# Performance work log

Measured on AMD Instinct MI355X. Metric: run time of the kernel, lower is better.

## Reference

```python
import jax, jax.numpy as jnp
import numpy as np
import math

EPS = 1e-6
N_HEADS = 16
THETA = 10000.0


def rms(x):
    # parameter-free RMSNorm: x * rsqrt(mean(x^2) + eps)
    return x * jax.lax.rsqrt(jnp.mean(x * x, axis=-1, keepdims=True) + EPS)


def silu(x):
    return x * jax.nn.sigmoid(x)


def rope_cos_sin(T, head_dim, theta):
    inv = 1.0 / (theta ** (jnp.arange(0, head_dim, 2, dtype=jnp.float32) / head_dim))
    freqs = jnp.arange(T, dtype=jnp.float32)[:, None] * inv[None, :]  # (T, head_dim/2)
    return jnp.cos(freqs), jnp.sin(freqs)


def apply_rope(x, cos, sin):
    # x: (B, H, T, dh); even/odd interleaved pairs as in torch reshape(...,-1,2).unbind(-1)
    x1 = x[..., 0::2]
    x2 = x[..., 1::2]
    o1 = x1 * cos - x2 * sin
    o2 = x1 * sin + x2 * cos
    return jnp.stack([o1, o2], axis=-1).reshape(x.shape)


def cache_linear(x, down, up):
    # x: (B,T,in), down: (h,in,c), up: (h,out,c) -> (B,T,out)
    a = jnp.einsum('bti,hic->bthc', x, down)
    a = jnp.einsum('bthc,hoc->btho', a, up)
    return rms(jnp.prod(a, axis=2))


def setup_inputs() -> dict:
    key = jax.random.key(0)
    ks = jax.random.split(key, 10)
    B, T, D = 1, 2048, 1024
    d_ff, ncb, cdim = 4096, 4, 64
    lin_std = math.sqrt(2.0 / (D + D))
    return {
        'x': jax.random.normal(ks[0], (B, T, D), jnp.float32),
        'ln1_w': jnp.ones((D,), jnp.float32),
        'ln2_w': jnp.ones((D,), jnp.float32),
        'wq': jax.random.normal(ks[1], (D, D), jnp.float32) * lin_std,
        'wk': jax.random.normal(ks[2], (D, D), jnp.float32) * lin_std,
        'wv': jax.random.normal(ks[3], (D, D), jnp.float32) * lin_std,
        'wo': jax.random.normal(ks[4], (D, D), jnp.float32) * lin_std,
        'w1_down': jax.random.normal(ks[5], (ncb, D, cdim), jnp.float32) * math.sqrt(2.0 / (D + cdim)),
        'w1_up': jax.random.normal(ks[6], (ncb, d_ff, cdim), jnp.float32) * math.sqrt(2.0 / (d_ff + cdim)),
        'w2_down': jax.random.normal(ks[7], (ncb, d_ff, cdim), jnp.float32) * math.sqrt(2.0 / (d_ff + cdim)),
        'w2_up': jax.random.normal(ks[8], (ncb, D, cdim), jnp.float32) * math.sqrt(2.0 / (D + cdim)),
    }


def reference(x, ln1_w, ln2_w, wq, wk, wv, wo, w1_down, w1_up, w2_down, w2_up):
    B, T, D = x.shape
    H = N_HEADS
    dh = D // H

    # --- attention sublayer (pre-RMSNorm) ---
    h = rms(x) * ln1_w
    def proj(w):
        return (h @ w.T).reshape(B, T, H, dh).transpose(0, 2, 1, 3)  # (B,H,T,dh)
    q, k, v = proj(wq), proj(wk), proj(wv)

    cos, sin = rope_cos_sin(T, dh, THETA)  # (T, dh/2)
    q = apply_rope(q, cos, sin)
    k = apply_rope(k, cos, sin)

    scores = jnp.einsum('bhid,bhjd->bhij', q, k) / math.sqrt(dh)
    causal = jnp.tril(jnp.ones((T, T), dtype=bool))
    scores = jnp.where(causal, scores, -jnp.inf)
    attn = jax.nn.softmax(scores, axis=-1)
    o = jnp.einsum('bhij,bhjd->bhid', attn, v)
    o = o.transpose(0, 2, 1, 3).reshape(B, T, D) @ wo.T
    x = x + o

    # --- CacheSiLU FFN sublayer (pre-RMSNorm) ---
    h2 = rms(x) * ln2_w
    a = cache_linear(h2, w1_down, w1_up)   # (B,T,d_ff)
    f = cache_linear(silu(a), w2_down, w2_up)  # (B,T,D)
    return x + f
```

## Files before the change

### kernel.cpp

```cpp
#include <hip/hip_runtime.h>
#include <math.h>
#include <stdint.h>

#define T_LEN   2048
#define D_MODEL 1024
#define NH      16
#define DFF     4096

typedef __attribute__((ext_vector_type(8))) short bf16x8;
typedef __attribute__((ext_vector_type(4))) float f32x4;
typedef __attribute__((ext_vector_type(4))) unsigned short u16x4;
typedef __attribute__((ext_vector_type(8))) unsigned short u16x8;
typedef unsigned short u16;

__device__ inline u16 f2b(float x) {
  unsigned int u = __float_as_uint(x);
  unsigned int r = (u + 0x7fffu + ((u >> 16) & 1u)) >> 16;
  return (u16)r;
}
__device__ inline float b2f(u16 h) { return __uint_as_float(((unsigned int)h) << 16); }

typedef const __attribute__((address_space(1))) unsigned int* gas_t;
typedef __attribute__((address_space(3))) unsigned int* las_t;
__device__ inline void gl_lds16(const void* g, void* l) {
  __builtin_amdgcn_global_load_lds((gas_t)g, (las_t)l, 16, 0, 0);
}

#define MFMA16(a, b, c) __builtin_amdgcn_mfma_f32_16x16x32_bf16((a), (b), (c), 0, 0, 0)

__global__ __launch_bounds__(256) void conv_bf16_kernel(
    const float* __restrict__ src, u16* __restrict__ dst, int n4) {
  int i = blockIdx.x * 256 + threadIdx.x;
  if (i < n4) {
    float4 v = reinterpret_cast<const float4*>(src)[i];
    u16x4 o = {f2b(v.x), f2b(v.y), f2b(v.z), f2b(v.w)};
    reinterpret_cast<u16x4*>(dst)[i] = o;
  }
}

__global__ __launch_bounds__(256) void conv4_kernel(
    const float* s0, const float* s1, const float* s2, const float* s3,
    u16* d0, u16* d1, u16* d2, u16* d3, int n4) {
  int z = blockIdx.z;
  const float* s = z == 0 ? s0 : (z == 1 ? s1 : (z == 2 ? s2 : s3));
  u16* d = z == 0 ? d0 : (z == 1 ? d1 : (z == 2 ? d2 : d3));
  int i = blockIdx.x * 256 + threadIdx.x;
  if (i < n4) {
    float4 v = reinterpret_cast<const float4*>(s)[i];
    u16x4 o = {f2b(v.x), f2b(v.y), f2b(v.z), f2b(v.w)};
    reinterpret_cast<u16x4*>(d)[i] = o;
  }
}

__global__ __launch_bounds__(256) void tr_kernel(
    const float* __restrict__ w, u16* __restrict__ wt, int K) {
  int k0 = blockIdx.x * 64, h = blockIdx.y;
  __shared__ float Ts[64][65];
  int tid = threadIdx.x;
#pragma unroll
  for (int i = 0; i < 4; ++i) {
    int idx = tid + i * 256;
    int r = idx >> 4, c4 = (idx & 15) * 4;
    float4 v = *reinterpret_cast<const float4*>(w + ((size_t)h * K + k0 + r) * 64 + c4);
    Ts[r][c4 + 0] = v.x; Ts[r][c4 + 1] = v.y; Ts[r][c4 + 2] = v.z; Ts[r][c4 + 3] = v.w;
  }
  __syncthreads();
#pragma unroll
  for (int i = 0; i < 4; ++i) {
    int idx = tid + i * 256;
    int c = idx >> 4, k4 = (idx & 15) * 4;
    u16x4 o = {f2b(Ts[k4 + 0][c]), f2b(Ts[k4 + 1][c]), f2b(Ts[k4 + 2][c]), f2b(Ts[k4 + 3][c])};
    *reinterpret_cast<u16x4*>(wt + (size_t)(h * 64 + c) * K + k0 + k4) = o;
  }
}

__global__ __launch_bounds__(256) void vtrans_kernel(
    const u16* __restrict__ V, u16* __restrict__ VT) {
  __shared__ u16 Ts[64][72];
  int t0 = blockIdx.x * 64, h = blockIdx.y;
  int tid = threadIdx.x;
#pragma unroll
  for (int it = 0; it < 2; ++it) {
    int c = tid + it * 256;
    int t = c >> 3, d8 = (c & 7) * 8;
    *reinterpret_cast<u16x8*>(&Ts[t][d8]) =
        *reinterpret_cast<const u16x8*>(V + (size_t)(t0 + t) * D_MODEL + h * 64 + d8);
  }
  __syncthreads();
#pragma unroll
  for (int it = 0; it < 2; ++it) {
    int c = tid + it * 256;
    int d = c >> 3, t8 = (c & 7) * 8;
    u16x8 o;
#pragma unroll
    for (int j = 0; j < 8; ++j) o[j] = Ts[t8 + j][d];
    *reinterpret_cast<u16x8*>(VT + ((size_t)h * 64 + d) * T_LEN + t0 + t8) = o;
  }
}

template <int NV, bool WEIGHT>
__global__ __launch_bounds__(256) void rms_bf16_kernel(
    const float* __restrict__ in, const float* __restrict__ w,
    u16* __restrict__ out, int width) {
  int row = blockIdx.x, tid = threadIdx.x;
  const float* rp = in + (size_t)row * width;
  float4 vals[NV];
  float ss = 0.f;
#pragma unroll
  for (int v = 0; v < NV; ++v) {
    vals[v] = reinterpret_cast<const float4*>(rp)[v * 256 + tid];
    ss += vals[v].x * vals[v].x + vals[v].y * vals[v].y +
          vals[v].z * vals[v].z + vals[v].w * vals[v].w;
  }
  for (int off = 32; off; off >>= 1) ss += __shfl_down(ss, off, 64);
  __shared__ float wsum[4];
  if ((tid & 63) == 0) wsum[tid >> 6] = ss;
  __syncthreads();
  float tot = wsum[0] + wsum[1] + wsum[2] + wsum[3];
  float scale = rsqrtf(tot / (float)width + 1e-6f);
#pragma unroll
  for (int v = 0; v < NV; ++v) {
    int c4 = v * 256 + tid;
    float o0 = vals[v].x * scale, o1 = vals[v].y * scale,
          o2 = vals[v].z * scale, o3 = vals[v].w * scale;
    if constexpr (WEIGHT) {
      float4 wv = reinterpret_cast<const float4*>(w)[c4];
      o0 *= wv.x; o1 *= wv.y; o2 *= wv.z; o3 *= wv.w;
    }
    u16x4 ov = {f2b(o0), f2b(o1), f2b(o2), f2b(o3)};
    reinterpret_cast<u16x4*>(out + (size_t)row * width)[c4] = ov;
  }
}

__global__ __launch_bounds__(256) void rms_silu_bf16_kernel(
    const u16* __restrict__ in, u16* __restrict__ out) {
  int row = blockIdx.x, tid = threadIdx.x;
  const u16* rp = in + (size_t)row * DFF;
  float f[16];
  float ss = 0.f;
#pragma unroll
  for (int v = 0; v < 2; ++v) {
    u16x8 c = reinterpret_cast<const u16x8*>(rp)[v * 256 + tid];
#pragma unroll
    for (int j = 0; j < 8; ++j) {
      float x = b2f((u16)c[j]);
      f[v * 8 + j] = x;
      ss += x * x;
    }
  }
  for (int off = 32; off; off >>= 1) ss += __shfl_down(ss, off, 64);
  __shared__ float wsum[4];
  if ((tid & 63) == 0) wsum[tid >> 6] = ss;
  __syncthreads();
  float tot = wsum[0] + wsum[1] + wsum[2] + wsum[3];
  float scale = rsqrtf(tot / (float)DFF + 1e-6f);
#pragma unroll
  for (int v = 0; v < 2; ++v) {
    u16x8 o;
#pragma unroll
    for (int j = 0; j < 8; ++j) {
      float x = f[v * 8 + j] * scale;
      x = x / (1.f + __expf(-x));
      o[j] = f2b(x);
    }
    reinterpret_cast<u16x8*>(out + (size_t)row * DFF)[v * 256 + tid] = o;
  }
}

__global__ __launch_bounds__(256) void rms_add_kernel(
    const float* __restrict__ in, const float* __restrict__ res,
    float* __restrict__ out) {
  int row = blockIdx.x, tid = threadIdx.x;
  float4 v = reinterpret_cast<const float4*>(in + (size_t)row * D_MODEL)[tid];
  float ss = v.x * v.x + v.y * v.y + v.z * v.z + v.w * v.w;
  for (int off = 32; off; off >>= 1) ss += __shfl_down(ss, off, 64);
  __shared__ float wsum[4];
  if ((tid & 63) == 0) wsum[tid >> 6] = ss;
  __syncthreads();
  float tot = wsum[0] + wsum[1] + wsum[2] + wsum[3];
  float scale = rsqrtf(tot / (float)D_MODEL + 1e-6f);
  float4 rv = reinterpret_cast<const float4*>(res + (size_t)row * D_MODEL)[tid];
  float4 o = make_float4(v.x * scale + rv.x, v.y * scale + rv.y,
                         v.z * scale + rv.z, v.w * scale + rv.w);
  reinterpret_cast<float4*>(out + (size_t)row * D_MODEL)[tid] = o;
}

template <int OUT>
__device__ inline void gemm_nt_body(const u16* A, const u16* B, void* Cv,
                                    const float* RES, int N, int lda, int Kloop,
                                    int row0, int col0) {
  __shared__ __align__(16) u16 As[128 * 32];
  __shared__ __align__(16) u16 Bs[128 * 32];
  int tid = threadIdx.x, lane = tid & 63, wid = tid >> 6;
  int wr = wid >> 1, wc = wid & 1;
  const f32x4 fz = {0.f, 0.f, 0.f, 0.f};
  f32x4 acc[4][4];
#pragma unroll
  for (int m = 0; m < 4; ++m)
#pragma unroll
    for (int n = 0; n < 4; ++n) acc[m][n] = fz;

  for (int k0 = 0; k0 < Kloop; k0 += 32) {
    __syncthreads();
#pragma unroll
    for (int i = 0; i < 2; ++i) {
      int wl = wid * 2 + i;
      int row = wl * 16 + (lane >> 2);
      int col8 = ((lane & 3) ^ (row & 3)) * 8;
      gl_lds16(A + (size_t)(row0 + row) * lda + k0 + col8, &As[wl * 512]);
      gl_lds16(B + (size_t)(col0 + row) * lda + k0 + col8, &Bs[wl * 512]);
    }
    __syncthreads();
    bf16x8 af[4], bfr[4];
#pragma unroll
    for (int m = 0; m < 4; ++m) {
      int r = wr * 64 + m * 16 + (lane & 15);
      af[m] = *reinterpret_cast<const bf16x8*>(&As[r * 32 + (((lane >> 4) ^ (r & 3)) << 3)]);
    }
#pragma unroll
    for (int n = 0; n < 4; ++n) {
      int r = wc * 64 + n * 16 + (lane & 15);
      bfr[n] = *reinterpret_cast<const bf16x8*>(&Bs[r * 32 + (((lane >> 4) ^ (r & 3)) << 3)]);
    }
#pragma unroll
    for (int m = 0; m < 4; ++m)
#pragma unroll
      for (int n = 0; n < 4; ++n) acc[m][n] = MFMA16(af[m], bfr[n], acc[m][n]);
  }
#pragma unroll
  for (int m = 0; m < 4; ++m)
#pragma unroll
    for (int n = 0; n < 4; ++n)
#pragma unroll
      for (int r = 0; r < 4; ++r) {
        int grow = row0 + wr * 64 + m * 16 + (lane >> 4) * 4 + r;
        int gcol = col0 + wc * 64 + n * 16 + (lane & 15);
        float v = acc[m][n][r];
        if constexpr (OUT == 0) {
          ((u16*)Cv)[(size_t)grow * N + gcol] = f2b(v);
        } else if constexpr (OUT == 1) {
          ((float*)Cv)[(size_t)grow * N + gcol] = v + RES[(size_t)grow * N + gcol];
        } else {
          ((float*)Cv)[(size_t)grow * N + gcol] = v;
        }
      }
}

__global__ __launch_bounds__(256) void gemm_qkv_kernel(
    const u16* __restrict__ A, const u16* Bq, const u16* Bk, const u16* Bv,
    u16* Cq, u16* Ck, u16* Cvp) {
  const u16* B = blockIdx.z == 0 ? Bq : (blockIdx.z == 1 ? Bk : Bv);
  u16* C = blockIdx.z == 0 ? Cq : (blockIdx.z == 1 ? Ck : Cvp);
  gemm_nt_body<0>(A, B, C, nullptr, D_MODEL, D_MODEL, D_MODEL,
                  blockIdx.y * 128, blockIdx.x * 128);
}
__global__ __launch_bounds__(256) void gemm_res_kernel(
    const u16* __restrict__ A, const u16* __restrict__ B, float* __restrict__ C,
    const float* __restrict__ RES) {
  gemm_nt_body<1>(A, B, C, RES, D_MODEL, D_MODEL, D_MODEL,
                  blockIdx.y * 128, blockIdx.x * 128);
}
__global__ __launch_bounds__(256) void gemm_splitk_kernel(
    const u16* __restrict__ A, const u16* __restrict__ B, float* __restrict__ Cp,
    int lda, int Kchunk) {
  int z = blockIdx.z;
  gemm_nt_body<2>(A + (size_t)z * Kchunk, B + (size_t)z * Kchunk,
                  Cp + (size_t)z * (T_LEN * 256), nullptr, 256, lda, Kchunk,
                  blockIdx.y * 128, blockIdx.x * 128);
}
__global__ __launch_bounds__(256) void reduce_conv_kernel(
    const float* __restrict__ part, u16* __restrict__ out, int n4, int nsplit) {
  int i = blockIdx.x * 256 + threadIdx.x;
  if (i >= n4) return;
  float4 a = reinterpret_cast<const float4*>(part)[i];
  for (int s = 1; s < nsplit; ++s) {
    float4 b = reinterpret_cast<const float4*>(part)[i + (size_t)s * n4];
    a.x += b.x; a.y += b.y; a.z += b.z; a.w += b.w;
  }
  u16x4 o = {f2b(a.x), f2b(a.y), f2b(a.z), f2b(a.w)};
  reinterpret_cast<u16x4*>(out)[i] = o;
}

template <bool BF16_OUT>
__global__ __launch_bounds__(256) void cache_up_mfma(
    const u16* __restrict__ Acoef, const u16* __restrict__ UP,
    void* __restrict__ Gv, int N) {
  __shared__ __align__(16) u16 As[128 * 64];
  __shared__ __align__(16) u16 Bs[128 * 64];
  int tid = threadIdx.x, lane = tid & 63, wid = tid >> 6;
  int wr = wid >> 1, wc = wid & 1;
  int row0 = blockIdx.y * 128, col0 = blockIdx.x * 128;
  const f32x4 fz = {0.f, 0.f, 0.f, 0.f};
  f32x4 prod[4][4];
#pragma unroll
  for (int m = 0; m < 4; ++m)
#pragma unroll
    for (int n = 0; n < 4; ++n) prod[m][n] = fz + 1.f;

  for (int h = 0; h < 4; ++h) {
    __syncthreads();
#pragma unroll
    for (int i = 0; i < 4; ++i) {
      int wl = wid * 4 + i;
      int row = wl * 8 + (lane >> 3);
      int col8 = ((lane & 7) ^ (row & 7)) * 8;
      gl_lds16(Acoef + (size_t)(row0 + row) * 256 + h * 64 + col8, &As[wl * 512]);
      gl_lds16(UP + ((size_t)h * N + col0 + row) * 64 + col8, &Bs[wl * 512]);
    }
    __syncthreads();
    f32x4 d[4][4];
#pragma unroll
    for (int m = 0; m < 4; ++m)
#pragma unroll
      for (int n = 0; n < 4; ++n) d[m][n] = fz;
#pragma unroll
    for (int kh = 0; kh < 2; ++kh) {
      bf16x8 af[4], bfr[4];
#pragma unroll
      for (int m = 0; m < 4; ++m) {
        int r = wr * 64 + m * 16 + (lane & 15);
        int slot = kh * 4 + (lane >> 4);
        af[m] = *reinterpret_cast<const bf16x8*>(&As[r * 64 + ((slot ^ (r & 7)) << 3)]);
      }
#pragma unroll
      for (int n = 0; n < 4; ++n) {
        int r = wc * 64 + n * 16 + (lane & 15);
        int slot = kh * 4 + (lane >> 4);
        bfr[n] = *reinterpret_cast<const bf16x8*>(&Bs[r * 64 + ((slot ^ (r & 7)) << 3)]);
      }
#pragma unroll
      for (int m = 0; m < 4; ++m)
#pragma unroll
        for (int n = 0; n < 4; ++n) d[m][n] = MFMA16(af[m], bfr[n], d[m][n]);
    }
#pragma unroll
    for (int m = 0; m < 4; ++m)
#pragma unroll
      for (int n = 0; n < 4; ++n) prod[m][n] *= d[m][n];
  }
#pragma unroll
  for (int m = 0; m < 4; ++m)
#pragma unroll
    for (int n = 0; n < 4; ++n)
#pragma unroll
      for (int r = 0; r < 4; ++r) {
        int grow = row0 + wr * 64 + m * 16 + (lane >> 4) * 4 + r;
        int gcol = col0 + wc * 64 + n * 16 + (lane & 15);
        if constexpr (BF16_OUT)
          ((u16*)Gv)[(size_t)grow * N + gcol] = f2b(prod[m][n][r]);
        else
          ((float*)Gv)[(size_t)grow * N + gcol] = prod[m][n][r];
      }
}

__global__ __launch_bounds__(256) void rope_bf16_kernel(u16* __restrict__ q,
                                                        u16* __restrict__ k) {
  int t = blockIdx.x, tid = threadIdx.x;
  const float NEG = -0.28782313662425573f;
#pragma unroll
  for (int u = 0; u < 2; ++u) {
    int p = tid + u * 256;
    int i = p & 31;
    int col = (p >> 5) * 64 + 2 * i;
    float ang = (float)t * __expf(NEG * (float)i);
    float sv, cv;
    __sincosf(ang, &sv, &cv);
    size_t idx = (size_t)t * D_MODEL + col;
    unsigned int* qp = reinterpret_cast<unsigned int*>(q + idx);
    unsigned int qv = *qp;
    float q1 = b2f(qv & 0xffff), q2 = b2f(qv >> 16);
    *qp = (unsigned int)f2b(q1 * cv - q2 * sv) |
          ((unsigned int)f2b(q1 * sv + q2 * cv) << 16);
    unsigned int* kp = reinterpret_cast<unsigned int*>(k + idx);
    unsigned int kv = *kp;
    float k1 = b2f(kv & 0xffff), k2 = b2f(kv >> 16);
    *kp = (unsigned int)f2b(k1 * cv - k2 * sv) |
          ((unsigned int)f2b(k1 * sv + k2 * cv) << 16);
  }
}

__global__ __launch_bounds__(128) void attn_mfma_kernel(
    const u16* __restrict__ Q, const u16* __restrict__ Kb,
    const u16* __restrict__ VT, u16* __restrict__ O) {
  __shared__ __align__(16) u16 Ks[64 * 64];
  __shared__ __align__(16) u16 Vt[64 * 64];
  int tid = threadIdx.x, lane = tid & 63, wid = tid >> 6;
  int G = lane >> 4, ql = lane & 15;
  int head = blockIdx.y, hoff = head * 64;
  int qt = (int)gridDim.x - 1 - (int)blockIdx.x;
  int q0 = qt * 32;
  int qg = q0 + wid * 16 + ql;

  bf16x8 aq[2];
  {
    const u16* qp = Q + (size_t)qg * D_MODEL + hoff + G * 8;
    aq[0] = *reinterpret_cast<const bf16x8*>(qp);
    aq[1] = *reinterpret_cast<const bf16x8*>(qp + 32);
  }
  const f32x4 fz = {0.f, 0.f, 0.f, 0.f};
  f32x4 accO[4];
#pragma unroll
  for (int n = 0; n < 4; ++n) accO[n] = fz;
  float m_p = -INFINITY, l_p = 0.f;

  int ntile = (q0 + 31) / 64 + 1;
  for (int jt = 0; jt < ntile; ++jt) {
    int j0 = jt * 64;
    __syncthreads();
#pragma unroll
    for (int i = 0; i < 4; ++i) {
      int wl = wid * 4 + i;
      int row = wl * 8 + (lane >> 3);
      int col8 = ((lane & 7) ^ (row & 7)) * 8;
      gl_lds16(Kb + (size_t)(j0 + row) * D_MODEL + hoff + col8, &Ks[wl * 512]);
      gl_lds16(VT + ((size_t)hoff + row) * T_LEN + j0 + col8, &Vt[wl * 512]);
    }
    __syncthreads();
    f32x4 s[4];
#pragma unroll
    for (int n = 0; n < 4; ++n) s[n] = fz;
#pragma unroll
    for (int n = 0; n < 4; ++n) {
      int kr = n * 16 + ql;
#pragma unroll
      for (int h = 0; h < 2; ++h) {
        int slot = (h * 4 + G) ^ (kr & 7);
        bf16x8 bk = *reinterpret_cast<const bf16x8*>(&Ks[kr * 64 + slot * 8]);
        s[n] = MFMA16(bk, aq[h], s[n]);
      }
    }
    bool diag = (jt == ntile - 1);
#pragma unroll
    for (int n = 0; n < 4; ++n)
#pragma unroll
      for (int r = 0; r < 4; ++r) {
        float sv = s[n][r] * 0.125f;
        if (diag && (j0 + n * 16 + 4 * G + r > qg)) sv = -INFINITY;
        s[n][r] = sv;
      }
    float mx = s[0][0];
#pragma unroll
    for (int n = 0; n < 4; ++n)
#pragma unroll
      for (int r = 0; r < 4; ++r) mx = fmaxf(mx, s[n][r]);
    mx = fmaxf(mx, __shfl_xor(mx, 16, 64));
    mx = fmaxf(mx, __shfl_xor(mx, 32, 64));
    float mn = fmaxf(m_p, mx);
    float rsc = __expf(m_p - mn);
    m_p = mn;
    float ls = 0.f;
#pragma unroll
    for (int n = 0; n < 4; ++n)
#pragma unroll
      for (int r = 0; r < 4; ++r) {
        float p = __expf(s[n][r] - mn);
        s[n][r] = p;
        ls += p;
      }
    ls += __shfl_xor(ls, 16, 64);
    ls += __shfl_xor(ls, 32, 64);
    l_p = l_p * rsc + ls;
    unsigned int w32[4][2];
#pragma unroll
    for (int n = 0; n < 4; ++n)
#pragma unroll
      for (int rr = 0; rr < 2; ++rr) {
        unsigned int pk;
        asm("v_cvt_pk_bf16_f32 %0, %1, %2"
            : "=v"(pk) : "v"(s[n][2 * rr]), "v"(s[n][2 * rr + 1]));
        w32[n][rr] = pk;
      }
    float rscx[4];
#pragma unroll
    for (int r = 0; r < 4; ++r) rscx[r] = __shfl(rsc, 4 * G + r, 64);
#pragma unroll
    for (int n = 0; n < 4; ++n)
#pragma unroll
      for (int r = 0; r < 4; ++r) accO[n][r] *= rscx[r];
#pragma unroll
    for (int kh = 0; kh < 2; ++kh) {
      union { unsigned int w[4]; bf16x8 v; } ap;
#pragma unroll
      for (int w = 0; w < 4; ++w) {
        int src = ql + (((2 * G + (w >> 1)) & 3) << 4);
        unsigned int v0 = (unsigned int)__shfl((int)w32[2 * kh][w & 1], src, 64);
        unsigned int v1 = (unsigned int)__shfl((int)w32[2 * kh + 1][w & 1], src, 64);
        ap.w[w] = (G >> 1) ? v1 : v0;
      }
#pragma unroll
      for (int n = 0; n < 4; ++n) {
        int d = n * 16 + ql;
        int slot = (kh * 4 + G) ^ (d & 7);
        bf16x8 bv = *reinterpret_cast<const bf16x8*>(&Vt[d * 64 + slot * 8]);
        accO[n] = MFMA16(ap.v, bv, accO[n]);
      }
    }
  }
  float invl = 1.f / l_p;
  float linvx[4];
#pragma unroll
  for (int r = 0; r < 4; ++r) linvx[r] = __shfl(invl, 4 * G + r, 64);
#pragma unroll
  for (int n = 0; n < 4; ++n)
#pragma unroll
    for (int r = 0; r < 4; ++r) {
      int qrow = q0 + wid * 16 + 4 * G + r;
      O[(size_t)qrow * D_MODEL + hoff + n * 16 + ql] = f2b(accO[n][r] * linvx[r]);
    }
}

extern "C" void kernel_launch(void* const* d_in, const int* in_sizes, int n_in,
                              void* d_out, int out_size, void* d_ws, size_t ws_size,
                              hipStream_t stream) {
  (void)in_sizes; (void)n_in; (void)out_size; (void)ws_size;
  const float* x   = (const float*)d_in[0];
  const float* ln1 = (const float*)d_in[1];
  const float* ln2 = (const float*)d_in[2];
  const float* wq  = (const float*)d_in[3];
  const float* wk  = (const float*)d_in[4];
  const float* wv  = (const float*)d_in[5];
  const float* wo  = (const float*)d_in[6];
  const float* w1d = (const float*)d_in[7];
  const float* w1u = (const float*)d_in[8];
  const float* w2d = (const float*)d_in[9];
  const float* w2u = (const float*)d_in[10];
  float* out = (float*)d_out;
  char* ws = (char*)d_ws;
  const size_t HMB = 1ull << 19;

  u16*   wqb  = (u16*)(ws + 0 * HMB);
  u16*   wkb  = (u16*)(ws + 4 * HMB);
  u16*   wvb  = (u16*)(ws + 8 * HMB);
  u16*   wob  = (u16*)(ws + 12 * HMB);
  u16*   w1ub = (u16*)(ws + 16 * HMB);
  u16*   w2ub = (u16*)(ws + 20 * HMB);
  u16*   wt1  = (u16*)(ws + 21 * HMB);
  u16*   wt2  = (u16*)(ws + 22 * HMB);
  u16*   hb   = (u16*)(ws + 26 * HMB);
  float* x1   = (float*)(ws + 34 * HMB);
  u16*   abuf = (u16*)(ws + 50 * HMB);
  u16*   qb   = (u16*)(ws + 52 * HMB);
  u16*   kb   = (u16*)(ws + 60 * HMB);
  u16*   vb   = (u16*)(ws + 68 * HMB);
  u16*   vtb  = (u16*)(ws + 76 * HMB);
  u16*   aob  = (u16*)(ws + 84 * HMB);
  u16*   g    = (u16*)(ws + 52 * HMB);
  float* g2   = (float*)(ws + 52 * HMB);
  u16*   sb   = (u16*)(ws + 84 * HMB);
  float* part = (float*)(ws + 116 * HMB);

  dim3 b256(256), b128(128);
  conv4_kernel<<<dim3(1024, 1, 4), b256, 0, stream>>>(wq, wk, wv, wo,
                                                      wqb, wkb, wvb, wob, 262144);
  conv_bf16_kernel<<<1024, b256, 0, stream>>>(w1u, w1ub, 262144);
  conv_bf16_kernel<<<256, b256, 0, stream>>>(w2u, w2ub, 65536);
  tr_kernel<<<dim3(16, 4), b256, 0, stream>>>(w1d, wt1, 1024);
  tr_kernel<<<dim3(64, 4), b256, 0, stream>>>(w2d, wt2, 4096);
  rms_bf16_kernel<1, true><<<T_LEN, b256, 0, stream>>>(x, ln1, hb, 1024);
  gemm_qkv_kernel<<<dim3(8, 16, 3), b256, 0, stream>>>(hb, wqb, wkb, wvb, qb, kb, vb);
  rope_bf16_kernel<<<T_LEN, b256, 0, stream>>>(qb, kb);
  vtrans_kernel<<<dim3(32, 16), b256, 0, stream>>>(vb, vtb);
  attn_mfma_kernel<<<dim3(T_LEN / 32, NH), b128, 0, stream>>>(qb, kb, vtb, aob);
  gemm_res_kernel<<<dim3(8, 16), b256, 0, stream>>>(aob, wob, x1, x);
  rms_bf16_kernel<1, true><<<T_LEN, b256, 0, stream>>>(x1, ln2, hb, 1024);
  gemm_splitk_kernel<<<dim3(2, 16, 4), b256, 0, stream>>>(hb, wt1, part, 1024, 256);
  reduce_conv_kernel<<<512, b256, 0, stream>>>(part, abuf, 131072, 4);
  cache_up_mfma<true><<<dim3(32, 16), b256, 0, stream>>>(abuf, w1ub, g, 4096);
  rms_silu_bf16_kernel<<<T_LEN, b256, 0, stream>>>(g, sb);
  gemm_splitk_kernel<<<dim3(2, 16, 8), b256, 0, stream>>>(sb, wt2, part, 4096, 512);
  reduce_conv_kernel<<<512, b256, 0, stream>>>(part, abuf, 131072, 8);
  cache_up_mfma<false><<<dim3(8, 16), b256, 0, stream>>>(abuf, w2ub, g2, 1024);
  rms_add_kernel<<<T_LEN, b256, 0, stream>>>(g2, x1, out);
}
```

Baseline: 280.9 us.

## Double-buffer LDS tiles in GEMM, cache-up and attention; enlarge attention blocks

Adds double-buffered shared-memory staging with explicit vmcnt waits to the GEMM body, the cache-up MFMA kernel and the attention kernel, so the next tile's global-to-LDS load overlaps the current tile's MFMA work. Attention blocks grow from 128 to 256 threads covering 64 query rows, which halves the block count and lets each K/V tile be reused by more waves. The three weight-conversion launches are merged into one kernel. The doubled LDS footprint may lower occupancy, and the larger attention tiles coarsen causal load balancing.

Measured after the change: 283.8 us. About the same (+1.0%).

```diff
diff --git a/kernel.cpp b/kernel.cpp
--- a/kernel.cpp
+++ b/kernel.cpp
@@ -27,23 +27,22 @@
 }
 
 #define MFMA16(a, b, c) __builtin_amdgcn_mfma_f32_16x16x32_bf16((a), (b), (c), 0, 0, 0)
-
-__global__ __launch_bounds__(256) void conv_bf16_kernel(
-    const float* __restrict__ src, u16* __restrict__ dst, int n4) {
-  int i = blockIdx.x * 256 + threadIdx.x;
-  if (i < n4) {
-    float4 v = reinterpret_cast<const float4*>(src)[i];
-    u16x4 o = {f2b(v.x), f2b(v.y), f2b(v.z), f2b(v.w)};
-    reinterpret_cast<u16x4*>(dst)[i] = o;
-  }
-}
-
-__global__ __launch_bounds__(256) void conv4_kernel(
+#define VMCNT(N) asm volatile("s_waitcnt vmcnt(" #N ")" ::: "memory")
+
+__global__ __launch_bounds__(256) void prep_conv_kernel(
     const float* s0, const float* s1, const float* s2, const float* s3,
-    u16* d0, u16* d1, u16* d2, u16* d3, int n4) {
+    const float* s4, const float* s5,
+    u16* d0, u16* d1, u16* d2, u16* d3, u16* d4, u16* d5) {
   int z = blockIdx.z;
-  const float* s = z == 0 ? s0 : (z == 1 ? s1 : (z == 2 ? s2 : s3));
-  u16* d = z == 0 ? d0 : (z == 1 ? d1 : (z == 2 ? d2 : d3));
+  const float* s; u16* d; int n4;
+  switch (z) {
+    case 0: s = s0; d = d0; n4 = 262144; break;
+    case 1: s = s1; d = d1; n4 = 262144; break;
+    case 2: s = s2; d = d2; n4 = 262144; break;
+    case 3: s = s3; d = d3; n4 = 262144; break;
+    case 4: s = s4; d = d4; n4 = 262144; break;
+    default: s = s5; d = d5; n4 = 65536; break;
+  }
   int i = blockIdx.x * 256 + threadIdx.x;
   if (i < n4) {
     float4 v = reinterpret_cast<const float4*>(s)[i];
@@ -189,8 +188,8 @@
 __device__ inline void gemm_nt_body(const u16* A, const u16* B, void* Cv,
                                     const float* RES, int N, int lda, int Kloop,
                                     int row0, int col0) {
-  __shared__ __align__(16) u16 As[128 * 32];
-  __shared__ __align__(16) u16 Bs[128 * 32];
+  __shared__ __align__(16) u16 As[2][128 * 32];
+  __shared__ __align__(16) u16 Bs[2][128 * 32];
   int tid = threadIdx.x, lane = tid & 63, wid = tid >> 6;
   int wr = wid >> 1, wc = wid & 1;
   const f32x4 fz = {0.f, 0.f, 0.f, 0.f};
@@ -200,32 +199,46 @@
 #pragma unroll
     for (int n = 0; n < 4; ++n) acc[m][n] = fz;
 
-  for (int k0 = 0; k0 < Kloop; k0 += 32) {
-    __syncthreads();
+  auto STAGE = [&](int buf, int k0) {
 #pragma unroll
     for (int i = 0; i < 2; ++i) {
       int wl = wid * 2 + i;
       int row = wl * 16 + (lane >> 2);
       int col8 = ((lane & 3) ^ (row & 3)) * 8;
-      gl_lds16(A + (size_t)(row0 + row) * lda + k0 + col8, &As[wl * 512]);
-      gl_lds16(B + (size_t)(col0 + row) * lda + k0 + col8, &Bs[wl * 512]);
+      gl_lds16(A + (size_t)(row0 + row) * lda + k0 + col8, &As[buf][wl * 512]);
+      gl_lds16(B + (size_t)(col0 + row) * lda + k0 + col8, &Bs[buf][wl * 512]);
+    }
+  };
+
+  STAGE(0, 0);
+  int nk = Kloop >> 5;
+  for (int j = 0; j < nk; ++j) {
+    int cur = j & 1;
+    if (j + 1 < nk) {
+      STAGE(cur ^ 1, (j + 1) * 32);
+      VMCNT(4);
+    } else {
+      VMCNT(0);
     }
     __syncthreads();
     bf16x8 af[4], bfr[4];
 #pragma unroll
     for (int m = 0; m < 4; ++m) {
       int r = wr * 64 + m * 16 + (lane & 15);
-      af[m] = *reinterpret_cast<const bf16x8*>(&As[r * 32 + (((lane >> 4) ^ (r & 3)) << 3)]);
+      af[m] = *reinterpret_cast<const bf16x8*>(
+          &As[cur][r * 32 + (((lane >> 4) ^ (r & 3)) << 3)]);
     }
 #pragma unroll
     for (int n = 0; n < 4; ++n) {
       int r = wc * 64 + n * 16 + (lane & 15);
-      bfr[n] = *reinterpret_cast<const bf16x8*>(&Bs[r * 32 + (((lane >> 4) ^ (r & 3)) << 3)]);
+      bfr[n] = *reinterpret_cast<const bf16x8*>(
+          &Bs[cur][r * 32 + (((lane >> 4) ^ (r & 3)) << 3)]);
     }
 #pragma unroll
     for (int m = 0; m < 4; ++m)
 #pragma unroll
       for (int n = 0; n < 4; ++n) acc[m][n] = MFMA16(af[m], bfr[n], acc[m][n]);
+    __syncthreads();
   }
 #pragma unroll
   for (int m = 0; m < 4; ++m)
@@ -285,8 +298,8 @@
 __global__ __launch_bounds__(256) void cache_up_mfma(
     const u16* __restrict__ Acoef, const u16* __restrict__ UP,
     void* __restrict__ Gv, int N) {
-  __shared__ __align__(16) u16 As[128 * 64];
-  __shared__ __align__(16) u16 Bs[128 * 64];
+  __shared__ __align__(16) u16 As[2][128 * 64];
+  __shared__ __align__(16) u16 Bs[2][128 * 64];
   int tid = threadIdx.x, lane = tid & 63, wid = tid >> 6;
   int wr = wid >> 1, wc = wid & 1;
   int row0 = blockIdx.y * 128, col0 = blockIdx.x * 128;
@@ -297,15 +310,25 @@
 #pragma unroll
     for (int n = 0; n < 4; ++n) prod[m][n] = fz + 1.f;
 
-  for (int h = 0; h < 4; ++h) {
-    __syncthreads();
+  auto STAGE = [&](int buf, int h) {
 #pragma unroll
     for (int i = 0; i < 4; ++i) {
       int wl = wid * 4 + i;
       int row = wl * 8 + (lane >> 3);
       int col8 = ((lane & 7) ^ (row & 7)) * 8;
-      gl_lds16(Acoef + (size_t)(row0 + row) * 256 + h * 64 + col8, &As[wl * 512]);
-      gl_lds16(UP + ((size_t)h * N + col0 + row) * 64 + col8, &Bs[wl * 512]);
+      gl_lds16(Acoef + (size_t)(row0 + row) * 256 + h * 64 + col8, &As[buf][wl * 512]);
+      gl_lds16(UP + ((size_t)h * N + col0 + row) * 64 + col8, &Bs[buf][wl * 512]);
+    }
+  };
+
+  STAGE(0, 0);
+  for (int h = 0; h < 4; ++h) {
+    int cur = h & 1;
+    if (h < 3) {
+      STAGE(cur ^ 1, h + 1);
+      VMCNT(8);
+    } else {
+      VMCNT(0);
     }
     __syncthreads();
     f32x4 d[4][4];
@@ -320,13 +343,15 @@
       for (int m = 0; m < 4; ++m) {
         int r = wr * 64 + m * 16 + (lane & 15);
         int slot = kh * 4 + (lane >> 4);
-        af[m] = *reinterpret_cast<const bf16x8*>(&As[r * 64 + ((slot ^ (r & 7)) << 3)]);
+        af[m] = *reinterpret_cast<const bf16x8*>(
+            &As[cur][r * 64 + ((slot ^ (r & 7)) << 3)]);
       }
 #pragma unroll
       for (int n = 0; n < 4; ++n) {
         int r = wc * 64 + n * 16 + (lane & 15);
         int slot = kh * 4 + (lane >> 4);
-        bfr[n] = *reinterpret_cast<const bf16x8*>(&Bs[r * 64 + ((slot ^ (r & 7)) << 3)]);
+        bfr[n] = *reinterpret_cast<const bf16x8*>(
+            &Bs[cur][r * 64 + ((slot ^ (r & 7)) << 3)]);
       }
 #pragma unroll
       for (int m = 0; m < 4; ++m)
@@ -337,6 +362,7 @@
     for (int m = 0; m < 4; ++m)
 #pragma unroll
       for (int n = 0; n < 4; ++n) prod[m][n] *= d[m][n];
+    __syncthreads();
   }
 #pragma unroll
   for (int m = 0; m < 4; ++m)
@@ -379,16 +405,16 @@
   }
 }
 
-__global__ __launch_bounds__(128) void attn_mfma_kernel(
+__global__ __launch_bounds__(256) void attn_mfma_kernel(
     const u16* __restrict__ Q, const u16* __restrict__ Kb,
     const u16* __restrict__ VT, u16* __restrict__ O) {
-  __shared__ __align__(16) u16 Ks[64 * 64];
-  __shared__ __align__(16) u16 Vt[64 * 64];
+  __shared__ __align__(16) u16 Ks[2][64 * 64];
+  __shared__ __align__(16) u16 Vt[2][64 * 64];
   int tid = threadIdx.x, lane = tid & 63, wid = tid >> 6;
   int G = lane >> 4, ql = lane & 15;
   int head = blockIdx.y, hoff = head * 64;
   int qt = (int)gridDim.x - 1 - (int)blockIdx.x;
-  int q0 = qt * 32;
+  int q0 = qt * 64;
   int qg = q0 + wid * 16 + ql;
 
   bf16x8 aq[2];
@@ -403,17 +429,27 @@
   for (int n = 0; n < 4; ++n) accO[n] = fz;
   float m_p = -INFINITY, l_p = 0.f;
 
-  int ntile = (q0 + 31) / 64 + 1;
+  auto STAGE = [&](int buf, int j0) {
+#pragma unroll
+    for (int i = 0; i < 2; ++i) {
+      int wl = wid * 2 + i;
+      int row = wl * 8 + (lane >> 3);
+      int col8 = ((lane & 7) ^ (row & 7)) * 8;
+      gl_lds16(Kb + (size_t)(j0 + row) * D_MODEL + hoff + col8, &Ks[buf][wl * 512]);
+      gl_lds16(VT + ((size_t)hoff + row) * T_LEN + j0 + col8, &Vt[buf][wl * 512]);
+    }
+  };
+
+  int ntile = qt + 1;
+  STAGE(0, 0);
   for (int jt = 0; jt < ntile; ++jt) {
     int j0 = jt * 64;
-    __syncthreads();
-#pragma unroll
-    for (int i = 0; i < 4; ++i) {
-      int wl = wid * 4 + i;
-      int row = wl * 8 + (lane >> 3);
-      int col8 = ((lane & 7) ^ (row & 7)) * 8;
-      gl_lds16(Kb + (size_t)(j0 + row) * D_MODEL + hoff + col8, &Ks[wl * 512]);
-      gl_lds16(VT + ((size_t)hoff + row) * T_LEN + j0 + col8, &Vt[wl * 512]);
+    int cur = jt & 1;
+    if (jt + 1 < ntile) {
+      STAGE(cur ^ 1, j0 + 64);
+      VMCNT(4);
+    } else {
+      VMCNT(0);
     }
     __syncthreads();
     f32x4 s[4];
@@ -425,7 +461,7 @@
 #pragma unroll
       for (int h = 0; h < 2; ++h) {
         int slot = (h * 4 + G) ^ (kr & 7);
-        bf16x8 bk = *reinterpret_cast<const bf16x8*>(&Ks[kr * 64 + slot * 8]);
+        bf16x8 bk = *reinterpret_cast<const bf16x8*>(&Ks[cur][kr * 64 + slot * 8]);
         s[n] = MFMA16(bk, aq[h], s[n]);
       }
     }
@@ -491,10 +527,11 @@
       for (int n = 0; n < 4; ++n) {
         int d = n * 16 + ql;
         int slot = (kh * 4 + G) ^ (d & 7);
-        bf16x8 bv = *reinterpret_cast<const bf16x8*>(&Vt[d * 64 + slot * 8]);
+        bf16x8 bv = *reinterpret_cast<const bf16x8*>(&Vt[cur][d * 64 + slot * 8]);
         accO[n] = MFMA16(ap.v, bv, accO[n]);
       }
     }
+    __syncthreads();
   }
   float invl = 1.f / l_p;
   float linvx[4];
@@ -549,18 +586,16 @@
   u16*   sb   = (u16*)(ws + 84 * HMB);
   float* part = (float*)(ws + 116 * HMB);
 
-  dim3 b256(256), b128(128);
-  conv4_kernel<<<dim3(1024, 1, 4), b256, 0, stream>>>(wq, wk, wv, wo,
-                                                      wqb, wkb, wvb, wob, 262144);
-  conv_bf16_kernel<<<1024, b256, 0, stream>>>(w1u, w1ub, 262144);
-  conv_bf16_kernel<<<256, b256, 0, stream>>>(w2u, w2ub, 65536);
+  dim3 b256(256);
+  prep_conv_kernel<<<dim3(1024, 1, 6), b256, 0, stream>>>(
+      wq, wk, wv, wo, w1u, w2u, wqb, wkb, wvb, wob, w1ub, w2ub);
   tr_kernel<<<dim3(16, 4), b256, 0, stream>>>(w1d, wt1, 1024);
   tr_kernel<<<dim3(64, 4), b256, 0, stream>>>(w2d, wt2, 4096);
   rms_bf16_kernel<1, true><<<T_LEN, b256, 0, stream>>>(x, ln1, hb, 1024);
   gemm_qkv_kernel<<<dim3(8, 16, 3), b256, 0, stream>>>(hb, wqb, wkb, wvb, qb, kb, vb);
   rope_bf16_kernel<<<T_LEN, b256, 0, stream>>>(qb, kb);
   vtrans_kernel<<<dim3(32, 16), b256, 0, stream>>>(vb, vtb);
-  attn_mfma_kernel<<<dim3(T_LEN / 32, NH), b128, 0, stream>>>(qb, kb, vtb, aob);
+  attn_mfma_kernel<<<dim3(T_LEN / 64, NH), b256, 0, stream>>>(qb, kb, vtb, aob);
   gemm_res_kernel<<<dim3(8, 16), b256, 0, stream>>>(aob, wob, x1, x);
   rms_bf16_kernel<1, true><<<T_LEN, b256, 0, stream>>>(x1, ln2, hb, 1024);
   gemm_splitk_kernel<<<dim3(2, 16, 4), b256, 0, stream>>>(hb, wt1, part, 1024, 256);
```
